# Optimization experiments

Measured on AMD Instinct MI355X. Metric: run time of the kernel, lower is better.

The kernel has to match this reference:

```python
import jax, jax.numpy as jnp
import numpy as np

D = 1024      # n_embd
H = 2048      # expert_hidden_dim
G = 4         # num_groups
EPG = 2       # experts_per_group
NH = 16       # num_heads
HD = D // NH  # head dim
L = 4         # num_layers
V = 32000     # vocab_size
NC = 32000    # num_classes
MAXS = 2048   # max_seq_len
B, S = 2, 1024
TEMP = 1.0    # router_temperature


def setup_inputs() -> dict:
    key = jax.random.key(0)
    ks = jax.random.split(key, 12)
    sc = 0.02
    def n(k, shape):
        return jax.random.normal(k, shape, jnp.float32) * sc
    return {
        "x": jax.random.randint(ks[0], (B, S), 0, V),
        "tok_emb": n(ks[1], (V, D)),
        "pos_emb": n(ks[2], (MAXS, D)),
        "in_proj_w": n(ks[3], (L, 3 * D, D)),
        "in_proj_b": jnp.zeros((L, 3 * D)),
        "out_w": n(ks[4], (L, D, D)),
        "out_b": jnp.zeros((L, D)),
        "ln1_w": jnp.ones((L, D)), "ln1_b": jnp.zeros((L, D)),
        "ln2_w": jnp.ones((L, D)), "ln2_b": jnp.zeros((L, D)),
        "gr_w": n(ks[5], (L, D, G)), "gr_b": jnp.zeros((L, G)),
        "er_w": n(ks[6], (L, G, D, EPG)), "er_b": jnp.zeros((L, G, EPG)),
        "w1": n(ks[7], (L, G, EPG, D, H)), "b1": jnp.zeros((L, G, EPG, H)),
        "w2": n(ks[8], (L, G, EPG, H, D)), "b2": jnp.zeros((L, G, EPG, D)),
        "lnf_w": jnp.ones((D,)), "lnf_b": jnp.zeros((D,)),
        "head_w": n(ks[9], (NC, D)), "head_b": jnp.zeros((NC,)),
    }


def _ln(x, w, b):
    m = x.mean(-1, keepdims=True)
    v = ((x - m) ** 2).mean(-1, keepdims=True)
    return (x - m) * jax.lax.rsqrt(v + 1e-5) * w + b


def _attn(x, wqkv, bqkv, wo, bo, mask):
    b, s, _ = x.shape
    qkv = x @ wqkv.T + bqkv
    q, k, v = jnp.split(qkv, 3, axis=-1)
    def heads(t):
        return t.reshape(b, s, NH, HD).transpose(0, 2, 1, 3)
    q, k, v = heads(q), heads(k), heads(v)
    sc = jnp.einsum('bhqd,bhkd->bhqk', q, k) / np.float32(np.sqrt(HD))
    sc = jnp.where(mask, sc, jnp.float32(-1e30))
    a = jax.nn.softmax(sc, axis=-1)
    o = jnp.einsum('bhqk,bhkd->bhqd', a, v).transpose(0, 2, 1, 3).reshape(b, s, D)
    return o @ wo.T + bo


def _moe(x, gw, gb, ew, eb, w1, b1, w2, b2):
    # x: [T, D] flattened tokens. 2-level routing: top-1 group, top-1 expert in group.
    gp = jax.nn.softmax((x @ gw + gb) / TEMP, axis=-1)                      # [T,G]
    gidx = jnp.argmax(gp, axis=-1)                                          # [T]
    ep = jax.nn.softmax((jnp.einsum('td,gde->tge', x, ew) + eb) / TEMP, -1)  # [T,G,EPG]
    ep_sel = jnp.take_along_axis(ep, gidx[:, None, None], axis=1)[:, 0]     # [T,EPG]
    eidx = jnp.argmax(ep_sel, axis=-1)                                      # [T]
    gate = (jnp.take_along_axis(gp, gidx[:, None], 1)[:, 0]
            * jnp.take_along_axis(ep_sel, eidx[:, None], 1)[:, 0])          # [T]
    hmid = jax.nn.relu(jnp.einsum('td,gedh->tgeh', x, w1) + b1)             # [T,G,EPG,H]
    out = jnp.einsum('tgeh,gehd->tged', hmid, w2) + b2                      # [T,G,EPG,D]
    comb = (jax.nn.one_hot(gidx, G, dtype=x.dtype)[:, :, None]
            * jax.nn.one_hot(eidx, EPG, dtype=x.dtype)[:, None, :]) * gate[:, None, None]
    return jnp.einsum('tge,tged->td', comb, out)


def reference(x, tok_emb, pos_emb, in_proj_w, in_proj_b, out_w, out_b,
              ln1_w, ln1_b, ln2_w, ln2_b, gr_w, gr_b, er_w, er_b,
              w1, b1, w2, b2, lnf_w, lnf_b, head_w, head_b):
    b, s = x.shape
    h = tok_emb[x] + pos_emb[jnp.arange(s)][None]
    mask = jnp.tril(jnp.ones((s, s), bool))
    for l in range(L):
        x1 = _ln(h, ln1_w[l], ln1_b[l])
        h = h + _attn(x1, in_proj_w[l], in_proj_b[l], out_w[l], out_b[l], mask)
        x2 = _ln(h, ln2_w[l], ln2_b[l]).reshape(b * s, D)
        h = h + _moe(x2, gr_w[l], gr_b[l], er_w[l], er_b[l],
                     w1[l], b1[l], w2[l], b2[l]).reshape(b, s, D)
    h = _ln(h, lnf_w, lnf_b).mean(axis=1)
    return h @ head_w.T + head_b
```

## Files before the change

kernel.cpp:

```cpp
#include <hip/hip_runtime.h>
#include <hip/hip_bf16.h>
#include <cstdint>
#include <cstddef>

#define D_   1024
#define H_   2048
#define G_   4
#define EPG_ 2
#define NE_  8
#define NH_  16
#define HD_  64
#define L_   4
#define V_   32000
#define NC_  32000
#define B_   2
#define S_   1024
#define T_   2048
#define MAXBLK_ 40
#define QB_  128

typedef __attribute__((__ext_vector_type__(8))) __bf16 bf16x8;
typedef __attribute__((__ext_vector_type__(4))) __bf16 bf16x4;
typedef __attribute__((__ext_vector_type__(4))) float  f32x4;

__device__ __forceinline__ void gl_lds16(const void* g, void* l) {
  __builtin_amdgcn_global_load_lds(
      (const __attribute__((address_space(1))) void*)g,
      (__attribute__((address_space(3))) void*)l, 16, 0, 0);
}

__device__ __forceinline__ float wave_sum(float v) {
  #pragma unroll
  for (int o = 32; o >= 1; o >>= 1) v += __shfl_xor(v, o, 64);
  return v;
}

__global__ __launch_bounds__(256) void embed_kernel(const int* __restrict__ x,
    const float* __restrict__ tok, const float* __restrict__ pos,
    float* __restrict__ h) {
  int t = blockIdx.x;
  int tid = threadIdx.x;
  int token = x[t];
  int s = t & (S_ - 1);
  float4 tv = *(const float4*)(tok + (size_t)token * D_ + tid * 4);
  float4 pv = *(const float4*)(pos + (size_t)s * D_ + tid * 4);
  float4 r;
  r.x = tv.x + pv.x; r.y = tv.y + pv.y; r.z = tv.z + pv.z; r.w = tv.w + pv.w;
  *(float4*)(h + (size_t)t * D_ + tid * 4) = r;
}

__device__ __forceinline__ float block_sum256(float v, float* sbuf) {
  v = wave_sum(v);
  int tid = threadIdx.x;
  if ((tid & 63) == 0) sbuf[tid >> 6] = v;
  __syncthreads();
  float r = sbuf[0] + sbuf[1] + sbuf[2] + sbuf[3];
  __syncthreads();
  return r;
}

template<bool F32OUT, bool BFOUT>
__global__ __launch_bounds__(256) void ln_kernel(const float* __restrict__ X,
    const float* __restrict__ w, const float* __restrict__ b,
    float* __restrict__ Yf, __bf16* __restrict__ Yb) {
  __shared__ float sbuf[4];
  int t = blockIdx.x, tid = threadIdx.x;
  const float* xr = X + (size_t)t * D_;
  float4 v = *(const float4*)(xr + tid * 4);
  float sum = v.x + v.y + v.z + v.w;
  float m = block_sum256(sum, sbuf) * (1.0f / D_);
  float dx = v.x - m, dy = v.y - m, dz = v.z - m, dw = v.w - m;
  float vs = dx * dx + dy * dy + dz * dz + dw * dw;
  float var = block_sum256(vs, sbuf) * (1.0f / D_);
  float rs = rsqrtf(var + 1e-5f);
  float4 wv = *(const float4*)(w + tid * 4);
  float4 bv = *(const float4*)(b + tid * 4);
  float4 o;
  o.x = dx * rs * wv.x + bv.x;
  o.y = dy * rs * wv.y + bv.y;
  o.z = dz * rs * wv.z + bv.z;
  o.w = dw * rs * wv.w + bv.w;
  if (F32OUT) *(float4*)(Yf + (size_t)t * D_ + tid * 4) = o;
  if (BFOUT) {
    bf16x4 ob = {(__bf16)o.x, (__bf16)o.y, (__bf16)o.z, (__bf16)o.w};
    *(bf16x4*)(Yb + (size_t)t * D_ + tid * 4) = ob;
  }
}

__global__ __launch_bounds__(256) void ln_route_kernel(const float* __restrict__ X,
    const float* __restrict__ lw, const float* __restrict__ lb,
    const float* __restrict__ gw, const float* __restrict__ gb,
    const float* __restrict__ ew, const float* __restrict__ eb,
    __bf16* __restrict__ Yb, int* __restrict__ eidx, float* __restrict__ gate) {
  int wv = threadIdx.x >> 6, lane = threadIdx.x & 63;
  int t = blockIdx.x * 4 + wv;
  const float* xr = X + (size_t)t * D_;
  float4 xv[4];
  #pragma unroll
  for (int k = 0; k < 4; k++) xv[k] = *(const float4*)(xr + lane * 4 + k * 256);
  float s = 0.f;
  #pragma unroll
  for (int k = 0; k < 4; k++) s += xv[k].x + xv[k].y + xv[k].z + xv[k].w;
  float m = wave_sum(s) * (1.0f / D_);
  float vs = 0.f;
  #pragma unroll
  for (int k = 0; k < 4; k++) {
    float a = xv[k].x - m, b2 = xv[k].y - m, c = xv[k].z - m, d = xv[k].w - m;
    vs += a * a + b2 * b2 + c * c + d * d;
  }
  float rs = rsqrtf(wave_sum(vs) * (1.0f / D_) + 1e-5f);
  float y[4][4];
  #pragma unroll
  for (int k = 0; k < 4; k++) {
    int d0 = lane * 4 + k * 256;
    float4 wv4 = *(const float4*)(lw + d0);
    float4 bv4 = *(const float4*)(lb + d0);
    y[k][0] = (xv[k].x - m) * rs * wv4.x + bv4.x;
    y[k][1] = (xv[k].y - m) * rs * wv4.y + bv4.y;
    y[k][2] = (xv[k].z - m) * rs * wv4.z + bv4.z;
    y[k][3] = (xv[k].w - m) * rs * wv4.w + bv4.w;
    bf16x4 ob = {(__bf16)y[k][0], (__bf16)y[k][1], (__bf16)y[k][2], (__bf16)y[k][3]};
    *(bf16x4*)(Yb + (size_t)t * D_ + d0) = ob;
  }
  float g0 = 0, g1 = 0, g2 = 0, g3 = 0;
  #pragma unroll
  for (int k = 0; k < 4; k++)
    #pragma unroll
    for (int j = 0; j < 4; j++) {
      int d = lane * 4 + k * 256 + j;
      float4 gv = *(const float4*)(gw + (size_t)d * G_);
      float yv = y[k][j];
      g0 += yv * gv.x; g1 += yv * gv.y; g2 += yv * gv.z; g3 += yv * gv.w;
    }
  g0 = wave_sum(g0) + gb[0];
  g1 = wave_sum(g1) + gb[1];
  g2 = wave_sum(g2) + gb[2];
  g3 = wave_sum(g3) + gb[3];
  float mx = fmaxf(fmaxf(g0, g1), fmaxf(g2, g3));
  float p0 = __expf(g0 - mx), p1 = __expf(g1 - mx), p2 = __expf(g2 - mx), p3 = __expf(g3 - mx);
  float psum = p0 + p1 + p2 + p3;
  int gidx = 0; float best = g0;
  if (g1 > best) { best = g1; gidx = 1; }
  if (g2 > best) { best = g2; gidx = 2; }
  if (g3 > best) { best = g3; gidx = 3; }
  float gpsel = ((gidx == 0) ? p0 : (gidx == 1) ? p1 : (gidx == 2) ? p2 : p3) / psum;
  const float* ewg = ew + (size_t)gidx * D_ * EPG_;
  float e0 = 0, e1 = 0;
  #pragma unroll
  for (int k = 0; k < 4; k++)
    #pragma unroll
    for (int j = 0; j < 4; j++) {
      int d = lane * 4 + k * 256 + j;
      float2 ev = *(const float2*)(ewg + (size_t)d * EPG_);
      e0 += y[k][j] * ev.x; e1 += y[k][j] * ev.y;
    }
  e0 = wave_sum(e0) + eb[gidx * EPG_ + 0];
  e1 = wave_sum(e1) + eb[gidx * EPG_ + 1];
  float em = fmaxf(e0, e1);
  float q0 = __expf(e0 - em), q1 = __expf(e1 - em);
  int ei = (e1 > e0) ? 1 : 0;
  float epsel = ((ei == 0) ? q0 : q1) / (q0 + q1);
  if (lane == 0) {
    eidx[t] = gidx * EPG_ + ei;
    gate[t] = gpsel * epsel;
  }
}

__global__ __launch_bounds__(256) void finalize_kernel(const int* __restrict__ eidx,
    int* __restrict__ counts, int* __restrict__ offs, int* __restrict__ tlist,
    int* __restrict__ blk) {
  __shared__ int hist[256][NE_];
  __shared__ int eoff[NE_];
  int tid = threadIdx.x;
  int loc[NE_];
  #pragma unroll
  for (int e = 0; e < NE_; e++) loc[e] = 0;
  int te[8];
  #pragma unroll
  for (int i = 0; i < 8; i++) { te[i] = eidx[tid * 8 + i]; loc[te[i]]++; }
  #pragma unroll
  for (int e = 0; e < NE_; e++) hist[tid][e] = loc[e];
  __syncthreads();
  for (int off = 1; off < 256; off <<= 1) {
    int v[NE_];
    #pragma unroll
    for (int e = 0; e < NE_; e++) v[e] = (tid >= off) ? hist[tid - off][e] : 0;
    __syncthreads();
    #pragma unroll
    for (int e = 0; e < NE_; e++) hist[tid][e] += v[e];
    __syncthreads();
  }
  if (tid == 0) {
    int acc = 0, nb = 0;
    for (int e = 0; e < NE_; e++) {
      int c = hist[255][e];
      eoff[e] = acc; counts[e] = c; offs[e] = acc; acc += c;
      for (int mt = 0; mt * 64 < c; mt++) blk[nb++] = e | (mt << 8);
    }
    for (; nb < MAXBLK_; nb++) blk[nb] = -1;
  }
  __syncthreads();
  int run[NE_];
  #pragma unroll
  for (int e = 0; e < NE_; e++) run[e] = eoff[e] + hist[tid][e] - loc[e];
  #pragma unroll
  for (int i = 0; i < 8; i++) {
    int e = te[i];
    tlist[run[e]++] = tid * 8 + i;
  }
}

template<int MODE, int NF, bool KN>
__global__ __launch_bounds__(256, 3) void gemm_mfma(
    const __bf16* __restrict__ A, const float* __restrict__ W,
    const float* __restrict__ bias, float* __restrict__ Cf,
    __bf16* __restrict__ Cb, const int* __restrict__ tlist,
    const int* __restrict__ offs, const int* __restrict__ counts,
    const float* __restrict__ gate, const int* __restrict__ blk,
    int N, int K) {
  __shared__ __bf16 As[2][64 * 64];
  __shared__ __bf16 Bs[2][NF * 32 * 64];
  int e = 0, mt = blockIdx.y, cnt = T_;
  if (MODE >= 2) {
    int bv = blk[blockIdx.y];
    if (bv < 0) return;
    e = bv & 255; mt = bv >> 8;
    cnt = counts[e];
  }
  int row0 = mt * 64;
  int lbase = (MODE >= 2) ? offs[e] : 0;
  int col0 = blockIdx.x * (NF * 32);
  const float* Wp = W + (size_t)e * N * K;
  const float* bp = bias + (size_t)e * N;
  int tid = threadIdx.x;
  int w = tid >> 6, lane = tid & 63, lq = lane & 15, lg = lane >> 4;
  int wr = w >> 1, wc = w & 1;

  const __bf16* asrc[2];
  #pragma unroll
  for (int it = 0; it < 2; it++) {
    int v = it * 256 + tid;
    int r = v >> 3, u = v & 7;
    int gr = row0 + r;
    long rowidx;
    if (MODE == 2) rowidx = tlist[lbase + ((gr < cnt) ? gr : cnt - 1)];
    else if (MODE == 3) rowidx = lbase + ((gr < cnt) ? gr : cnt - 1);
    else rowidx = gr;
    asrc[it] = A + (size_t)rowidx * K + (u ^ (r & 7)) * 8;
  }
  const float* bsrc[NF];
  int bdst[NF];
  #pragma unroll
  for (int it = 0; it < NF; it++) {
    if (!KN) {
      int v = it * 256 + tid;
      int n = v >> 3, u = v & 7;
      bsrc[it] = Wp + (size_t)(col0 + n) * K + u * 8;
      bdst[it] = n * 64 + (u ^ (n & 7)) * 8;
    } else {
      int v = it * 256 + tid;
      int n = v & (NF * 32 - 1), u = v / (NF * 32);
      bsrc[it] = Wp + (size_t)(u * 8) * N + col0 + n;
      bdst[it] = n * 64 + (u ^ (n & 7)) * 8;
    }
  }

  float brp[NF * 8];
  f32x4 acc[2][NF] = {};

  auto loadB = [&](int k0) {
    #pragma unroll
    for (int it = 0; it < NF; it++) {
      if (!KN) {
        float4 f0 = *(const float4*)(bsrc[it] + k0);
        float4 f1 = *(const float4*)(bsrc[it] + k0 + 4);
        brp[it * 8 + 0] = f0.x; brp[it * 8 + 1] = f0.y;
        brp[it * 8 + 2] = f0.z; brp[it * 8 + 3] = f0.w;
        brp[it * 8 + 4] = f1.x; brp[it * 8 + 5] = f1.y;
        brp[it * 8 + 6] = f1.z; brp[it * 8 + 7] = f1.w;
      } else {
        #pragma unroll
        for (int j = 0; j < 8; j++)
          brp[it * 8 + j] = bsrc[it][(size_t)(k0 + j) * N];
      }
    }
  };
  auto writeB = [&](int buf) {
    #pragma unroll
    for (int it = 0; it < NF; it++) {
      bf16x8 bb = {(__bf16)brp[it * 8 + 0], (__bf16)brp[it * 8 + 1],
                   (__bf16)brp[it * 8 + 2], (__bf16)brp[it * 8 + 3],
                   (__bf16)brp[it * 8 + 4], (__bf16)brp[it * 8 + 5],
                   (__bf16)brp[it * 8 + 6], (__bf16)brp[it * 8 + 7]};
      *(bf16x8*)&Bs[buf][bdst[it]] = bb;
    }
  };
  auto stageA = [&](int buf, int k0) {
    #pragma unroll
    for (int it = 0; it < 2; it++)
      gl_lds16(asrc[it] + k0, &As[buf][(it * 256 + tid) * 8]);
  };
  auto mfmaPhase = [&](int buf) {
    __builtin_amdgcn_s_setprio(1);
    #pragma unroll
    for (int kk = 0; kk < 2; kk++) {
      bf16x8 a[2], b[NF];
      int us = ((lg + kk * 4) ^ (lq & 7)) * 8;
      #pragma unroll
      for (int fi = 0; fi < 2; fi++)
        a[fi] = *(const bf16x8*)&As[buf][(wr * 32 + fi * 16 + lq) * 64 + us];
      #pragma unroll
      for (int fj = 0; fj < NF; fj++)
        b[fj] = *(const bf16x8*)&Bs[buf][(wc * (NF * 16) + fj * 16 + lq) * 64 + us];
      #pragma unroll
      for (int fi = 0; fi < 2; fi++)
        #pragma unroll
        for (int fj = 0; fj < NF; fj++)
          acc[fi][fj] = __builtin_amdgcn_mfma_f32_16x16x32_bf16(a[fi], b[fj], acc[fi][fj], 0, 0, 0);
    }
    __builtin_amdgcn_s_setprio(0);
  };

  loadB(0);
  stageA(0, 0);
  writeB(0);
  __syncthreads();

  int buf = 0;
  for (int k0 = 0; k0 < K; k0 += 64) {
    int nk = k0 + 64;
    if (nk < K) {
      stageA(buf ^ 1, nk);
      loadB(nk);
    }
    mfmaPhase(buf);
    if (nk < K) writeB(buf ^ 1);
    __syncthreads();
    buf ^= 1;
  }

  #pragma unroll
  for (int fi = 0; fi < 2; fi++) {
    #pragma unroll
    for (int v = 0; v < 4; v++) {
      int r = row0 + wr * 32 + fi * 16 + lg * 4 + v;
      long orow;
      float gv = 1.f;
      if (MODE >= 2) {
        if (r >= cnt) continue;
        if (MODE == 2) orow = lbase + r;
        else { orow = tlist[lbase + r]; gv = gate[orow]; }
      } else {
        orow = r;
      }
      #pragma unroll
      for (int fj = 0; fj < NF; fj++) {
        int c = col0 + wc * (NF * 16) + fj * 16 + lq;
        float val = acc[fi][fj][v] + bp[c];
        if (MODE == 0)      Cb[orow * N + c] = (__bf16)val;
        else if (MODE == 1) Cf[orow * N + c] += val;
        else if (MODE == 2) Cb[orow * N + c] = (__bf16)fmaxf(val, 0.f);
        else                Cf[orow * N + c] += gv * val;
      }
    }
  }
}

#define SC_LOG2 0.18033688011112042f
__global__ __launch_bounds__(512) void attn_mfma_kernel(const __bf16* __restrict__ qkv,
                                                        __bf16* __restrict__ out) {
  __shared__ __bf16 Ks[64][72];
  __shared__ __bf16 Vt[64][72];
  __shared__ __bf16 Ps[QB_][72];
  int tid = threadIdx.x;
  int w = tid >> 6, lane = tid & 63, lq = lane & 15, lg = lane >> 4;
  int qt = (S_ / QB_ - 1) - blockIdx.x;
  int b = blockIdx.y >> 4, hh = blockIdx.y & 15;
  const __bf16* qbase = qkv + (size_t)b * S_ * 3 * D_ + hh * HD_;

  bf16x8 qa[2];
  {
    const __bf16* qp = qbase + (size_t)(qt * QB_ + w * 16 + lq) * 3 * D_ + lg * 8;
    qa[0] = *(const bf16x8*)qp;
    qa[1] = *(const bf16x8*)(qp + 32);
  }

  f32x4 o[4] = {};
  float m_[4] = {-1e30f, -1e30f, -1e30f, -1e30f};
  float l_[4] = {0.f, 0.f, 0.f, 0.f};

  int rowmin = qt * QB_ + w * 16;
  int srow = tid >> 3, sc8 = tid & 7;
  int nkt = qt * 2 + 2;

  for (int kt = 0; kt < nkt; kt++) {
    {
      const __bf16* kp = qbase + (size_t)(kt * 64 + srow) * 3 * D_ + D_ + sc8 * 8;
      *(bf16x8*)&Ks[srow][sc8 * 8] = *(const bf16x8*)kp;
      bf16x8 vv = *(const bf16x8*)(kp + D_);
      int cs = srow ^ (sc8 << 3);
      #pragma unroll
      for (int j = 0; j < 8; j++) Vt[sc8 * 8 + j][cs] = vv[j];
    }
    __syncthreads();

    if (kt * 64 <= rowmin + 15) {
      f32x4 s[4] = {};
      #pragma unroll
      for (int kk = 0; kk < 2; kk++)
        #pragma unroll
        for (int fc = 0; fc < 4; fc++) {
          bf16x8 kf = *(const bf16x8*)&Ks[fc * 16 + lq][lg * 8 + kk * 32];
          s[fc] = __builtin_amdgcn_mfma_f32_16x16x32_bf16(qa[kk], kf, s[fc], 0, 0, 0);
        }

      bool need_mask = (kt * 64 + 63 > rowmin);
      #pragma unroll
      for (int fc = 0; fc < 4; fc++)
        #pragma unroll
        for (int v = 0; v < 4; v++) {
          float sv = s[fc][v] * SC_LOG2;
          if (need_mask && (kt * 64 + fc * 16 + lq) > (rowmin + lg * 4 + v)) sv = -1e30f;
          s[fc][v] = sv;
        }

      #pragma unroll
      for (int v = 0; v < 4; v++) {
        float rm = fmaxf(fmaxf(s[0][v], s[1][v]), fmaxf(s[2][v], s[3][v]));
        #pragma unroll
        for (int o2 = 8; o2 >= 1; o2 >>= 1) rm = fmaxf(rm, __shfl_xor(rm, o2, 64));
        if (rm > m_[v]) {
          float cc = exp2f(m_[v] - rm);
          m_[v] = rm;
          l_[v] *= cc;
          o[0][v] *= cc; o[1][v] *= cc; o[2][v] *= cc; o[3][v] *= cc;
        }
        float rs = 0.f;
        #pragma unroll
        for (int fc = 0; fc < 4; fc++) {
          float p = exp2f(s[fc][v] - m_[v]);
          s[fc][v] = p; rs += p;
        }
        l_[v] += rs;
        #pragma unroll
        for (int fc = 0; fc < 4; fc++)
          Ps[w * 16 + lg * 4 + v][fc * 16 + lq] = (__bf16)s[fc][v];
      }
      asm volatile("" ::: "memory");

      #pragma unroll
      for (int kk = 0; kk < 2; kk++) {
        bf16x8 pa = *(const bf16x8*)&Ps[w * 16 + lq][lg * 8 + kk * 32];
        #pragma unroll
        for (int dc = 0; dc < 4; dc++) {
          int d = dc * 16 + lq;
          int col = (lg * 8 + kk * 32) ^ ((d >> 3) << 3);
          bf16x8 vb = *(const bf16x8*)&Vt[d][col];
          o[dc] = __builtin_amdgcn_mfma_f32_16x16x32_bf16(pa, vb, o[dc], 0, 0, 0);
        }
      }
    }
    __syncthreads();
  }

  #pragma unroll
  for (int v = 0; v < 4; v++) {
    float ls = l_[v];
    #pragma unroll
    for (int o2 = 8; o2 >= 1; o2 >>= 1) ls += __shfl_xor(ls, o2, 64);
    float inv = 1.0f / ls;
    int row = rowmin + lg * 4 + v;
    __bf16* op = out + ((size_t)b * S_ + row) * D_ + hh * HD_;
    #pragma unroll
    for (int dc = 0; dc < 4; dc++)
      op[dc * 16 + lq] = (__bf16)(o[dc][v] * inv);
  }
}

__global__ __launch_bounds__(256) void mean_part_kernel(const float* __restrict__ X,
                                                        float* __restrict__ part) {
  int bd = blockIdx.x * 256 + threadIdx.x;
  int chunk = blockIdx.y;
  int b = bd >> 10, d = bd & 1023;
  float s = 0.f;
  #pragma unroll 4
  for (int i = 0; i < 64; i++) {
    int sidx = chunk * 64 + i;
    s += X[((size_t)b * S_ + sidx) * D_ + d];
  }
  part[chunk * T_ + bd] = s;
}

__global__ __launch_bounds__(256) void mean_final_kernel(const float* __restrict__ part,
                                                         float* __restrict__ hm) {
  int bd = blockIdx.x * 256 + threadIdx.x;
  float s = 0.f;
  #pragma unroll
  for (int c = 0; c < 16; c++) s += part[c * T_ + bd];
  hm[bd] = s * (1.0f / S_);
}

__global__ __launch_bounds__(256) void head_kernel(const float* __restrict__ hm,
    const float* __restrict__ hw, const float* __restrict__ hb,
    float* __restrict__ out) {
  int w = threadIdx.x >> 6;
  int lane = threadIdx.x & 63;
  int c = blockIdx.x * 4 + w;
  const float* row = hw + (size_t)c * D_;
  float acc0 = 0.f, acc1 = 0.f;
  #pragma unroll
  for (int k = 0; k < 4; k++) {
    int d = lane * 4 + k * 256;
    float4 wv = *(const float4*)(row + d);
    float4 h0 = *(const float4*)(hm + d);
    float4 h1 = *(const float4*)(hm + D_ + d);
    acc0 += wv.x * h0.x + wv.y * h0.y + wv.z * h0.z + wv.w * h0.w;
    acc1 += wv.x * h1.x + wv.y * h1.y + wv.z * h1.z + wv.w * h1.w;
  }
  #pragma unroll
  for (int o = 32; o >= 1; o >>= 1) {
    acc0 += __shfl_xor(acc0, o, 64);
    acc1 += __shfl_xor(acc1, o, 64);
  }
  if (lane == 0) {
    float bias = hb[c];
    out[c] = acc0 + bias;
    out[NC_ + c] = acc1 + bias;
  }
}

extern "C" void kernel_launch(void* const* d_in, const int* in_sizes, int n_in,
                              void* d_out, int out_size, void* d_ws, size_t ws_size,
                              hipStream_t stream) {
  const int*   x        = (const int*)d_in[0];
  const float* tok_emb  = (const float*)d_in[1];
  const float* pos_emb  = (const float*)d_in[2];
  const float* in_proj_w= (const float*)d_in[3];
  const float* in_proj_b= (const float*)d_in[4];
  const float* out_w    = (const float*)d_in[5];
  const float* out_b    = (const float*)d_in[6];
  const float* ln1_w    = (const float*)d_in[7];
  const float* ln1_b    = (const float*)d_in[8];
  const float* ln2_w    = (const float*)d_in[9];
  const float* ln2_b    = (const float*)d_in[10];
  const float* gr_w     = (const float*)d_in[11];
  const float* gr_b     = (const float*)d_in[12];
  const float* er_w     = (const float*)d_in[13];
  const float* er_b     = (const float*)d_in[14];
  const float* w1       = (const float*)d_in[15];
  const float* b1       = (const float*)d_in[16];
  const float* w2       = (const float*)d_in[17];
  const float* b2       = (const float*)d_in[18];
  const float* lnf_w    = (const float*)d_in[19];
  const float* lnf_b    = (const float*)d_in[20];
  const float* head_w   = (const float*)d_in[21];
  const float* head_b   = (const float*)d_in[22];

  char* wp = (char*)d_ws;
  auto carve = [&](size_t bytes) -> char* {
    char* p = wp;
    wp += (bytes + 255) & ~(size_t)255;
    return p;
  };
  float*  h      = (float*)carve((size_t)T_ * D_ * 4);
  float*  x1     = (float*)carve((size_t)T_ * D_ * 4);
  __bf16* x1b    = (__bf16*)carve((size_t)T_ * D_ * 2);
  __bf16* qkvb   = (__bf16*)carve((size_t)T_ * 3 * D_ * 2);
  __bf16* attnb  = (__bf16*)carve((size_t)T_ * D_ * 2);
  __bf16* hmidb  = (__bf16*)carve((size_t)T_ * H_ * 2);
  float*  part   = (float*)carve((size_t)16 * T_ * 4);
  float*  hm     = (float*)carve((size_t)B_ * D_ * 4);
  float*  gate   = (float*)carve((size_t)T_ * 4);
  int*    eidx   = (int*)carve((size_t)T_ * 4);
  int*    tlist  = (int*)carve((size_t)T_ * 4);
  int*    counts = (int*)carve(64);
  int*    offs   = (int*)carve(64);
  int*    blk    = (int*)carve(MAXBLK_ * 4);

  embed_kernel<<<T_, 256, 0, stream>>>(x, tok_emb, pos_emb, h);

  for (int l = 0; l < L_; l++) {
    ln_kernel<false, true><<<T_, 256, 0, stream>>>(h, ln1_w + l * D_, ln1_b + l * D_,
                                                   nullptr, x1b);
    gemm_mfma<0, 4, false><<<dim3(24, 32, 1), 256, 0, stream>>>(
        x1b, in_proj_w + (size_t)l * 3 * D_ * D_, in_proj_b + (size_t)l * 3 * D_,
        nullptr, qkvb, nullptr, nullptr, nullptr, nullptr, nullptr, 3 * D_, D_);
    attn_mfma_kernel<<<dim3(S_ / QB_, B_ * NH_), 512, 0, stream>>>(qkvb, attnb);
    gemm_mfma<1, 2, false><<<dim3(16, 32, 1), 256, 0, stream>>>(
        attnb, out_w + (size_t)l * D_ * D_, out_b + (size_t)l * D_, h, nullptr,
        nullptr, nullptr, nullptr, nullptr, nullptr, D_, D_);

    ln_route_kernel<<<T_ / 4, 256, 0, stream>>>(h,
        ln2_w + l * D_, ln2_b + l * D_,
        gr_w + (size_t)l * D_ * G_, gr_b + (size_t)l * G_,
        er_w + (size_t)l * G_ * D_ * EPG_, er_b + (size_t)l * G_ * EPG_,
        x1b, eidx, gate);
    finalize_kernel<<<1, 256, 0, stream>>>(eidx, counts, offs, tlist, blk);

    gemm_mfma<2, 4, true><<<dim3(H_ / 128, MAXBLK_, 1), 256, 0, stream>>>(
        x1b, w1 + (size_t)l * NE_ * D_ * H_, b1 + (size_t)l * NE_ * H_, nullptr, hmidb,
        tlist, offs, counts, nullptr, blk, H_, D_);
    gemm_mfma<3, 2, true><<<dim3(D_ / 64, MAXBLK_, 1), 256, 0, stream>>>(
        hmidb, w2 + (size_t)l * NE_ * H_ * D_, b2 + (size_t)l * NE_ * D_, h, nullptr,
        tlist, offs, counts, gate, blk, D_, H_);
  }

  ln_kernel<true, false><<<T_, 256, 0, stream>>>(h, lnf_w, lnf_b, x1, nullptr);
  mean_part_kernel<<<dim3(B_ * D_ / 256, 16), 256, 0, stream>>>(x1, part);
  mean_final_kernel<<<B_ * D_ / 256, 256, 0, stream>>>(part, hm);
  head_kernel<<<NC_ / 4, 256, 0, stream>>>(hm, head_w, head_b, (float*)d_out);
}
```

Measured before the change: 860.8 us.

## Fuse routing finalize into last LN-route block; shrink attention query tile to 64

The separate single-block finalize kernel is removed. Its histogram, scan and token-list build now run in whichever ln_route block finishes last, detected with a global atomic counter, which saves one launch per layer. The attention kernel drops from 128-query tiles with 512 threads to 64-query tiles with 256 threads. That doubles the grid for causal load balance and removes the per-wave skip branch, at the cost of reloading K/V into more blocks. Correctness of the last-block path depends on threadfence ordering between blocks.

```diff
diff --git a/kernel.cpp b/kernel.cpp
--- a/kernel.cpp
+++ b/kernel.cpp
@@ -17,7 +17,6 @@
 #define S_   1024
 #define T_   2048
 #define MAXBLK_ 40
-#define QB_  128
 
 typedef __attribute__((__ext_vector_type__(8))) __bf16 bf16x8;
 typedef __attribute__((__ext_vector_type__(4))) __bf16 bf16x4;
@@ -37,9 +36,10 @@
 
 __global__ __launch_bounds__(256) void embed_kernel(const int* __restrict__ x,
     const float* __restrict__ tok, const float* __restrict__ pos,
-    float* __restrict__ h) {
+    float* __restrict__ h, int* __restrict__ counter) {
   int t = blockIdx.x;
   int tid = threadIdx.x;
+  if (t == 0 && tid == 0) counter[0] = 0;
   int token = x[t];
   int s = t & (S_ - 1);
   float4 tv = *(const float4*)(tok + (size_t)token * D_ + tid * 4);
@@ -91,7 +91,12 @@
     const float* __restrict__ lw, const float* __restrict__ lb,
     const float* __restrict__ gw, const float* __restrict__ gb,
     const float* __restrict__ ew, const float* __restrict__ eb,
-    __bf16* __restrict__ Yb, int* __restrict__ eidx, float* __restrict__ gate) {
+    __bf16* __restrict__ Yb, int* __restrict__ eidx, float* __restrict__ gate,
+    int* __restrict__ counter, int* __restrict__ counts, int* __restrict__ offs,
+    int* __restrict__ tlist, int* __restrict__ blk) {
+  __shared__ int hist[256][NE_];
+  __shared__ int eoff[NE_];
+  __shared__ int lastflag;
   int wv = threadIdx.x >> 6, lane = threadIdx.x & 63;
   int t = blockIdx.x * 4 + wv;
   const float* xr = X + (size_t)t * D_;
@@ -164,13 +169,16 @@
     eidx[t] = gidx * EPG_ + ei;
     gate[t] = gpsel * epsel;
   }
-}
-
-__global__ __launch_bounds__(256) void finalize_kernel(const int* __restrict__ eidx,
-    int* __restrict__ counts, int* __restrict__ offs, int* __restrict__ tlist,
-    int* __restrict__ blk) {
-  __shared__ int hist[256][NE_];
-  __shared__ int eoff[NE_];
+  __syncthreads();
+  if (threadIdx.x == 0) {
+    __threadfence();
+    int arr = atomicAdd(counter, 1);
+    lastflag = (arr == (int)gridDim.x - 1);
+  }
+  __syncthreads();
+  if (!lastflag) return;
+
+  __threadfence();
   int tid = threadIdx.x;
   int loc[NE_];
   #pragma unroll
@@ -182,12 +190,12 @@
   for (int e = 0; e < NE_; e++) hist[tid][e] = loc[e];
   __syncthreads();
   for (int off = 1; off < 256; off <<= 1) {
-    int v[NE_];
-    #pragma unroll
-    for (int e = 0; e < NE_; e++) v[e] = (tid >= off) ? hist[tid - off][e] : 0;
+    int v2[NE_];
+    #pragma unroll
+    for (int e = 0; e < NE_; e++) v2[e] = (tid >= off) ? hist[tid - off][e] : 0;
     __syncthreads();
     #pragma unroll
-    for (int e = 0; e < NE_; e++) hist[tid][e] += v[e];
+    for (int e = 0; e < NE_; e++) hist[tid][e] += v2[e];
     __syncthreads();
   }
   if (tid == 0) {
@@ -198,6 +206,7 @@
       for (int mt = 0; mt * 64 < c; mt++) blk[nb++] = e | (mt << 8);
     }
     for (; nb < MAXBLK_; nb++) blk[nb] = -1;
+    counter[0] = 0;
   }
   __syncthreads();
   int run[NE_];
@@ -367,20 +376,20 @@
 }
 
 #define SC_LOG2 0.18033688011112042f
-__global__ __launch_bounds__(512) void attn_mfma_kernel(const __bf16* __restrict__ qkv,
+__global__ __launch_bounds__(256) void attn_mfma_kernel(const __bf16* __restrict__ qkv,
                                                         __bf16* __restrict__ out) {
   __shared__ __bf16 Ks[64][72];
   __shared__ __bf16 Vt[64][72];
-  __shared__ __bf16 Ps[QB_][72];
+  __shared__ __bf16 Ps[64][72];
   int tid = threadIdx.x;
   int w = tid >> 6, lane = tid & 63, lq = lane & 15, lg = lane >> 4;
-  int qt = (S_ / QB_ - 1) - blockIdx.x;
+  int qt = (S_ / 64 - 1) - blockIdx.x;
   int b = blockIdx.y >> 4, hh = blockIdx.y & 15;
   const __bf16* qbase = qkv + (size_t)b * S_ * 3 * D_ + hh * HD_;
 
   bf16x8 qa[2];
   {
-    const __bf16* qp = qbase + (size_t)(qt * QB_ + w * 16 + lq) * 3 * D_ + lg * 8;
+    const __bf16* qp = qbase + (size_t)(qt * 64 + w * 16 + lq) * 3 * D_ + lg * 8;
     qa[0] = *(const bf16x8*)qp;
     qa[1] = *(const bf16x8*)(qp + 32);
   }
@@ -389,12 +398,13 @@
   float m_[4] = {-1e30f, -1e30f, -1e30f, -1e30f};
   float l_[4] = {0.f, 0.f, 0.f, 0.f};
 
-  int rowmin = qt * QB_ + w * 16;
-  int srow = tid >> 3, sc8 = tid & 7;
-  int nkt = qt * 2 + 2;
-
-  for (int kt = 0; kt < nkt; kt++) {
-    {
+  int rowmin = qt * 64 + w * 16;
+
+  for (int kt = 0; kt <= qt; kt++) {
+    #pragma unroll
+    for (int it = 0; it < 2; it++) {
+      int idx = tid + it * 256;
+      int srow = idx >> 3, sc8 = idx & 7;
       const __bf16* kp = qbase + (size_t)(kt * 64 + srow) * 3 * D_ + D_ + sc8 * 8;
       *(bf16x8*)&Ks[srow][sc8 * 8] = *(const bf16x8*)kp;
       bf16x8 vv = *(const bf16x8*)(kp + D_);
@@ -404,60 +414,58 @@
     }
     __syncthreads();
 
-    if (kt * 64 <= rowmin + 15) {
-      f32x4 s[4] = {};
-      #pragma unroll
-      for (int kk = 0; kk < 2; kk++)
-        #pragma unroll
-        for (int fc = 0; fc < 4; fc++) {
-          bf16x8 kf = *(const bf16x8*)&Ks[fc * 16 + lq][lg * 8 + kk * 32];
-          s[fc] = __builtin_amdgcn_mfma_f32_16x16x32_bf16(qa[kk], kf, s[fc], 0, 0, 0);
-        }
-
-      bool need_mask = (kt * 64 + 63 > rowmin);
+    f32x4 s[4] = {};
+    #pragma unroll
+    for (int kk = 0; kk < 2; kk++)
+      #pragma unroll
+      for (int fc = 0; fc < 4; fc++) {
+        bf16x8 kf = *(const bf16x8*)&Ks[fc * 16 + lq][lg * 8 + kk * 32];
+        s[fc] = __builtin_amdgcn_mfma_f32_16x16x32_bf16(qa[kk], kf, s[fc], 0, 0, 0);
+      }
+
+    bool need_mask = (kt == qt);
+    #pragma unroll
+    for (int fc = 0; fc < 4; fc++)
+      #pragma unroll
+      for (int v = 0; v < 4; v++) {
+        float sv = s[fc][v] * SC_LOG2;
+        if (need_mask && (fc * 16 + lq) > (w * 16 + lg * 4 + v)) sv = -1e30f;
+        s[fc][v] = sv;
+      }
+
+    #pragma unroll
+    for (int v = 0; v < 4; v++) {
+      float rm = fmaxf(fmaxf(s[0][v], s[1][v]), fmaxf(s[2][v], s[3][v]));
+      #pragma unroll
+      for (int o2 = 8; o2 >= 1; o2 >>= 1) rm = fmaxf(rm, __shfl_xor(rm, o2, 64));
+      if (rm > m_[v]) {
+        float cc = exp2f(m_[v] - rm);
+        m_[v] = rm;
+        l_[v] *= cc;
+        o[0][v] *= cc; o[1][v] *= cc; o[2][v] *= cc; o[3][v] *= cc;
+      }
+      float rs = 0.f;
+      #pragma unroll
+      for (int fc = 0; fc < 4; fc++) {
+        float p = exp2f(s[fc][v] - m_[v]);
+        s[fc][v] = p; rs += p;
+      }
+      l_[v] += rs;
       #pragma unroll
       for (int fc = 0; fc < 4; fc++)
-        #pragma unroll
-        for (int v = 0; v < 4; v++) {
-          float sv = s[fc][v] * SC_LOG2;
-          if (need_mask && (kt * 64 + fc * 16 + lq) > (rowmin + lg * 4 + v)) sv = -1e30f;
-          s[fc][v] = sv;
-        }
-
-      #pragma unroll
-      for (int v = 0; v < 4; v++) {
-        float rm = fmaxf(fmaxf(s[0][v], s[1][v]), fmaxf(s[2][v], s[3][v]));
-        #pragma unroll
-        for (int o2 = 8; o2 >= 1; o2 >>= 1) rm = fmaxf(rm, __shfl_xor(rm, o2, 64));
-        if (rm > m_[v]) {
-          float cc = exp2f(m_[v] - rm);
-          m_[v] = rm;
-          l_[v] *= cc;
-          o[0][v] *= cc; o[1][v] *= cc; o[2][v] *= cc; o[3][v] *= cc;
-        }
-        float rs = 0.f;
-        #pragma unroll
-        for (int fc = 0; fc < 4; fc++) {
-          float p = exp2f(s[fc][v] - m_[v]);
-          s[fc][v] = p; rs += p;
-        }
-        l_[v] += rs;
-        #pragma unroll
-        for (int fc = 0; fc < 4; fc++)
-          Ps[w * 16 + lg * 4 + v][fc * 16 + lq] = (__bf16)s[fc][v];
-      }
-      asm volatile("" ::: "memory");
-
-      #pragma unroll
-      for (int kk = 0; kk < 2; kk++) {
-        bf16x8 pa = *(const bf16x8*)&Ps[w * 16 + lq][lg * 8 + kk * 32];
-        #pragma unroll
-        for (int dc = 0; dc < 4; dc++) {
-          int d = dc * 16 + lq;
-          int col = (lg * 8 + kk * 32) ^ ((d >> 3) << 3);
-          bf16x8 vb = *(const bf16x8*)&Vt[d][col];
-          o[dc] = __builtin_amdgcn_mfma_f32_16x16x32_bf16(pa, vb, o[dc], 0, 0, 0);
-        }
+        Ps[w * 16 + lg * 4 + v][fc * 16 + lq] = (__bf16)s[fc][v];
+    }
+    asm volatile("" ::: "memory");
+
+    #pragma unroll
+    for (int kk = 0; kk < 2; kk++) {
+      bf16x8 pa = *(const bf16x8*)&Ps[w * 16 + lq][lg * 8 + kk * 32];
+      #pragma unroll
+      for (int dc = 0; dc < 4; dc++) {
+        int d = dc * 16 + lq;
+        int col = (lg * 8 + kk * 32) ^ ((d >> 3) << 3);
+        bf16x8 vb = *(const bf16x8*)&Vt[d][col];
+        o[dc] = __builtin_amdgcn_mfma_f32_16x16x32_bf16(pa, vb, o[dc], 0, 0, 0);
       }
     }
     __syncthreads();
@@ -576,8 +584,9 @@
   int*    counts = (int*)carve(64);
   int*    offs   = (int*)carve(64);
   int*    blk    = (int*)carve(MAXBLK_ * 4);
-
-  embed_kernel<<<T_, 256, 0, stream>>>(x, tok_emb, pos_emb, h);
+  int*    counter= (int*)carve(64);
+
+  embed_kernel<<<T_, 256, 0, stream>>>(x, tok_emb, pos_emb, h, counter);
 
   for (int l = 0; l < L_; l++) {
     ln_kernel<false, true><<<T_, 256, 0, stream>>>(h, ln1_w + l * D_, ln1_b + l * D_,
@@ -585,7 +594,7 @@
     gemm_mfma<0, 4, false><<<dim3(24, 32, 1), 256, 0, stream>>>(
         x1b, in_proj_w + (size_t)l * 3 * D_ * D_, in_proj_b + (size_t)l * 3 * D_,
         nullptr, qkvb, nullptr, nullptr, nullptr, nullptr, nullptr, 3 * D_, D_);
-    attn_mfma_kernel<<<dim3(S_ / QB_, B_ * NH_), 512, 0, stream>>>(qkvb, attnb);
+    attn_mfma_kernel<<<dim3(S_ / 64, B_ * NH_), 256, 0, stream>>>(qkvb, attnb);
     gemm_mfma<1, 2, false><<<dim3(16, 32, 1), 256, 0, stream>>>(
         attnb, out_w + (size_t)l * D_ * D_, out_b + (size_t)l * D_, h, nullptr,
         nullptr, nullptr, nullptr, nullptr, nullptr, D_, D_);
@@ -594,8 +603,7 @@
         ln2_w + l * D_, ln2_b + l * D_,
         gr_w + (size_t)l * D_ * G_, gr_b + (size_t)l * G_,
         er_w + (size_t)l * G_ * D_ * EPG_, er_b + (size_t)l * G_ * EPG_,
-        x1b, eidx, gate);
-    finalize_kernel<<<1, 256, 0, stream>>>(eidx, counts, offs, tlist, blk);
+        x1b, eidx, gate, counter, counts, offs, tlist, blk);
 
     gemm_mfma<2, 4, true><<<dim3(H_ / 128, MAXBLK_, 1), 256, 0, stream>>>(
         x1b, w1 + (size_t)l * NE_ * D_ * H_, b1 + (size_t)l * NE_ * H_, nullptr, hmidb,
```

Measured after the change: 891.7 us. 1.04x slower.
